# Kernel optimization log

Measured on AMD Instinct MI355X. Metric: run time of the kernel, lower is better.

## Reference

```python
import jax, jax.numpy as jnp
import numpy as np

N_NODES = 50000  # 4 node types x 12500
N_PER = 12500
E = 600000
H = 128
IN_DIMS = [128, 128, 64, 64]


def setup_inputs() -> dict:
    key = jax.random.key(0)
    ks = jax.random.split(key, 16)
    inp = {}
    for i, d in enumerate(IN_DIMS):
        inp[f"feat{i}"] = jax.random.normal(ks[i], (N_PER, d), dtype=jnp.float32)
        # xavier_normal-ish init, gain 1.414
        std = 1.414 * np.sqrt(2.0 / (d + H))
        inp[f"W_fc{i}"] = jax.random.normal(ks[4 + i], (d, H), dtype=jnp.float32) * std
        inp[f"b_fc{i}"] = jnp.zeros((H,), dtype=jnp.float32)
    inp["src"] = jax.random.randint(ks[8], (E,), 0, N_NODES, dtype=jnp.int32)
    inp["dst"] = jax.random.randint(ks[9], (E,), 0, N_NODES, dtype=jnp.int32)
    inp["e_feat"] = jax.random.randint(ks[10], (E,), 0, 36, dtype=jnp.int32)
    inp["b_g0"] = jnp.zeros((H,), dtype=jnp.float32)  # GraphConv layer0 (weight=False, bias)
    inp["W_g1"] = jax.random.normal(ks[11], (H, H), dtype=jnp.float32) * np.sqrt(1.0 / H)
    inp["b_g1"] = jnp.zeros((H,), dtype=jnp.float32)
    return inp


def _degree_norms(src, dst):
    ones = jnp.ones((src.shape[0],), dtype=jnp.float32)
    deg_out = jax.ops.segment_sum(ones, src, num_segments=N_NODES)
    deg_in = jax.ops.segment_sum(ones, dst, num_segments=N_NODES)
    # DGL norm='both': D_out^{-1/2} on src side, D_in^{-1/2} on dst side (clamp 0-degree)
    out_norm = jax.lax.rsqrt(jnp.maximum(deg_out, 1.0))
    in_norm = jax.lax.rsqrt(jnp.maximum(deg_in, 1.0))
    return out_norm, in_norm


def _gcn_aggregate(h, src, dst, out_norm, in_norm):
    m = (h * out_norm[:, None])[src]                      # [E, H] gather
    agg = jax.ops.segment_sum(m, dst, num_segments=N_NODES)
    return agg * in_norm[:, None]


def reference(feat0, feat1, feat2, feat3,
              W_fc0, b_fc0, W_fc1, b_fc1, W_fc2, b_fc2, W_fc3, b_fc3,
              src, dst, e_feat, b_g0, W_g1, b_g1):
    # per-node-type linear projections, then concat along node dim
    h = jnp.concatenate([
        feat0 @ W_fc0 + b_fc0,
        feat1 @ W_fc1 + b_fc1,
        feat2 @ W_fc2 + b_fc2,
        feat3 @ W_fc3 + b_fc3,
    ], axis=0)  # [N_NODES, H]

    out_norm, in_norm = _degree_norms(src, dst)
    # GraphConv layer 0: weight=False, bias, activation (dropout p=0 -> identity)
    h = jax.nn.relu(_gcn_aggregate(h, src, dst, out_norm, in_norm) + b_g0)
    # GraphConv layer 1: aggregate, then linear weight + bias, activation
    h = jax.nn.relu(_gcn_aggregate(h, src, dst, out_norm, in_norm) @ W_g1 + b_g1)

    e = e_feat.astype(jnp.float32)  # e_feat.reshape(-1,1).float() in original
    # forward graph: msg = ft + sum_{r in 0..4} where(e==r, ft, 0) = ft * (1 + 1{e in 0..4})
    w_fwd = 1.0 + sum((e == float(r)).astype(jnp.float32) for r in (0, 1, 2, 3, 4))
    agg_a = jax.ops.segment_sum(h[src] * w_fwd[:, None], dst, num_segments=N_NODES)
    # transpose graph (reversed edges, same e): msg = sum_{r in {6,14,30}} where(e==r, ft, 0)
    w_bwd = sum((e == float(r)).astype(jnp.float32) for r in (6, 14, 30))
    agg_b = jax.ops.segment_sum(h[dst] * w_bwd[:, None], src, num_segments=N_NODES)
    return agg_a + agg_b
```

## Files before the change

kernel.cpp:

```cpp
#include <hip/hip_runtime.h>
#include <hip/hip_bf16.h>

#define N_NODES 50000
#define N_PER   12500
#define E_EDGES 600000
#define HDIM    128

#define NBLK_FC    ((N_PER + 63) / 64)
#define NBLK_G     ((N_NODES + 63) / 64)
#define NBLK_NODE  ((N_NODES + 255) / 256)
#define MASK31  0x7fffffff

#define HQD 64
#define HSL_D (E_EDGES / HQD)
#define NBLK_DB (HQD * 4)
#define HQS 32
#define HSL_S (E_EDGES / HQS)
#define NBLK_S (HQS * 4)

typedef __attribute__((ext_vector_type(8))) short bfrag;
typedef __attribute__((ext_vector_type(4))) float ffrag;

__device__ __forceinline__ unsigned short f2bf(float f) {
    union { float f; unsigned u; } x; x.f = f;
    unsigned r = x.u + 0x7fffu + ((x.u >> 16) & 1u);
    return (unsigned short)(r >> 16);
}
__device__ __forceinline__ float lo_bf(unsigned v) { return __uint_as_float(v << 16); }
__device__ __forceinline__ float hi_bf(unsigned v) { return __uint_as_float(v & 0xffff0000u); }
__device__ __forceinline__ unsigned pack2(float a, float b) {
    return (unsigned)f2bf(a) | ((unsigned)f2bf(b) << 16);
}
__device__ __forceinline__ float onrm_of(int deg) {
    return rsqrtf(fmaxf((float)deg, 1.0f));
}

__device__ __forceinline__ void acc8_add(float* acc, uint4 v) {
    acc[0] += lo_bf(v.x); acc[1] += hi_bf(v.x);
    acc[2] += lo_bf(v.y); acc[3] += hi_bf(v.y);
    acc[4] += lo_bf(v.z); acc[5] += hi_bf(v.z);
    acc[6] += lo_bf(v.w); acc[7] += hi_bf(v.w);
}
__device__ __forceinline__ void acc8_addw(float* acc, uint4 v, float w) {
    acc[0] += lo_bf(v.x) * w; acc[1] += hi_bf(v.x) * w;
    acc[2] += lo_bf(v.y) * w; acc[3] += hi_bf(v.y) * w;
    acc[4] += lo_bf(v.z) * w; acc[5] += hi_bf(v.z) * w;
    acc[6] += lo_bf(v.w) * w; acc[7] += hi_bf(v.w) * w;
}

__global__ __launch_bounds__(256) void prep_kernel(
    const float* __restrict__ W0, const float* __restrict__ W1,
    const float* __restrict__ W2, const float* __restrict__ W3,
    const float* __restrict__ Wg,
    const int* __restrict__ src, const int* __restrict__ dst,
    const int* __restrict__ ef,
    unsigned short* __restrict__ Wp,
    unsigned short* __restrict__ partialS,
    unsigned short* __restrict__ partialD,
    unsigned char*  __restrict__ partialB) {
    __shared__ unsigned hist[N_PER];
    int b = blockIdx.x;
    if (b < NBLK_DB) {
        const int q = b >> 2;
        const int p = b & 3;
        const int g0 = p * N_PER;
        for (int j = threadIdx.x; j < N_PER; j += 256) hist[j] = 0;
        __syncthreads();
        const int e0 = q * HSL_D;
        for (int i = e0 + threadIdx.x; i < e0 + HSL_D; i += 256) {
            int d = dst[i], t = ef[i], s = src[i];
            unsigned rd = (unsigned)(d - g0);
            if (rd < (unsigned)N_PER) atomicAdd(&hist[rd], 1u);
            if (t == 6 || t == 14 || t == 30) {
                unsigned rs = (unsigned)(s - g0);
                if (rs < (unsigned)N_PER) atomicAdd(&hist[rs], 0x10000u);
            }
        }
        __syncthreads();
        for (int j = threadIdx.x; j < N_PER; j += 256) {
            unsigned h = hist[j];
            partialD[(size_t)q * N_NODES + g0 + j] = (unsigned short)(h & 0xffffu);
            partialB[(size_t)q * N_NODES + g0 + j] = (unsigned char)(h >> 16);
        }
    } else if (b < NBLK_DB + NBLK_S) {
        const int r = b - NBLK_DB;
        const int q = r >> 2;
        const int p = r & 3;
        const int g0 = p * N_PER;
        for (int j = threadIdx.x; j < N_PER; j += 256) hist[j] = 0;
        __syncthreads();
        const int e0 = q * HSL_S;
        for (int i = e0 + threadIdx.x; i < e0 + HSL_S; i += 256) {
            unsigned rr = (unsigned)(src[i] - g0);
            if (rr < (unsigned)N_PER) atomicAdd(&hist[rr], 1u);
        }
        __syncthreads();
        for (int j = threadIdx.x; j < N_PER; j += 256)
            partialS[(size_t)q * N_NODES + g0 + j] = (unsigned short)hist[j];
    } else {
        int tid = (b - (NBLK_DB + NBLK_S)) * 256 + threadIdx.x;
        const float* W; int D, base, off;
        if      (tid < 2048) { W = W0; D = 128; base = 0;    off = 0;     }
        else if (tid < 4096) { W = W1; D = 128; base = 2048; off = 16384; }
        else if (tid < 5120) { W = W2; D = 64;  base = 4096; off = 32768; }
        else if (tid < 6144) { W = W3; D = 64;  base = 5120; off = 40960; }
        else                 { W = Wg; D = 128; base = 6144; off = 49152; }
        int t2 = tid - base;
        int KT = D / 32;
        int l = t2 & 63;
        int tt = t2 >> 6;
        int kt = tt % KT, n0 = tt / KT;
        int n = n0 * 16 + (l & 15);
        int kb = kt * 32 + (l >> 4) * 8;
#pragma unroll
        for (int j = 0; j < 8; ++j)
            Wp[(size_t)off + (size_t)t2 * 8 + j] = f2bf(W[(size_t)(kb + j) * 128 + n]);
    }
}

__global__ __launch_bounds__(256) void plane_prefix_kernel(
    unsigned short* __restrict__ partialD, unsigned char* __restrict__ partialB,
    const unsigned short* __restrict__ partialS,
    int* __restrict__ degD, int* __restrict__ degB,
    int* __restrict__ scanD, int* __restrict__ scanB,
    int* __restrict__ blocksumD, int* __restrict__ blocksumB,
    float* __restrict__ onrm_buf) {
    const int t = threadIdx.x;
    const int n = blockIdx.x * 256 + t;
    int dD = 0, dB = 0;
    if (n < N_NODES) {
        int run = 0;
#pragma unroll
        for (int q = 0; q < HQD; ++q) {
            size_t ix = (size_t)q * N_NODES + n;
            int c = partialD[ix];
            partialD[ix] = (unsigned short)run;
            run += c;
        }
        dD = run; degD[n] = run;
        run = 0;
#pragma unroll
        for (int q = 0; q < HQD; ++q) {
            size_t ix = (size_t)q * N_NODES + n;
            int c = partialB[ix];
            partialB[ix] = (unsigned char)run;
            run += c;
        }
        dB = run; degB[n] = run;
        int dS = 0;
#pragma unroll
        for (int q = 0; q < HQS; ++q)
            dS += partialS[(size_t)q * N_NODES + n];
        onrm_buf[n] = onrm_of(dS);
    }
    __shared__ int sD[256], sB[256];
    sD[t] = dD; sB[t] = dB;
    __syncthreads();
    for (int off = 1; off < 256; off <<= 1) {
        int xD = (t >= off) ? sD[t - off] : 0;
        int xB = (t >= off) ? sB[t - off] : 0;
        __syncthreads();
        sD[t] += xD; sB[t] += xB;
        __syncthreads();
    }
    if (n < N_NODES) {
        scanD[n] = sD[t] - dD;
        scanB[n] = sB[t] - dB;
    }
    if (t == 255) {
        blocksumD[blockIdx.x] = sD[255];
        blocksumB[blockIdx.x] = sB[255];
    }
}

__global__ __launch_bounds__(256) void base_add_kernel(
    const int* __restrict__ blocksumD, const int* __restrict__ blocksumB,
    int* __restrict__ scanD, int* __restrict__ scanB) {
    __shared__ int sD[256], sB[256];
    const int t = threadIdx.x;
    const int bid = blockIdx.x;
    sD[t] = (t < bid) ? blocksumD[t] : 0;
    sB[t] = (t < bid) ? blocksumB[t] : 0;
    __syncthreads();
    for (int off = 128; off >= 1; off >>= 1) {
        if (t < off) { sD[t] += sD[t + off]; sB[t] += sB[t + off]; }
        __syncthreads();
    }
    const int n = bid * 256 + t;
    if (n < N_NODES) { scanD[n] += sD[0]; scanB[n] += sB[0]; }
}

__global__ __launch_bounds__(1024) void scatter_kernel(
    const int* __restrict__ src, const int* __restrict__ dst,
    const int* __restrict__ ef,
    const unsigned short* __restrict__ prefD,
    const unsigned char*  __restrict__ prefB,
    const int* __restrict__ scanD, const int* __restrict__ scanB,
    int* __restrict__ bucket, int* __restrict__ bucketB)
{
    __shared__ unsigned offP[N_PER];
    const int b = blockIdx.x;
    const int q = b >> 2;
    const int p = b & 3;
    const int g0 = p * N_PER;
    for (int j = threadIdx.x; j < N_PER; j += 1024)
        offP[j] = (unsigned)(scanD[g0 + j] + (int)prefD[(size_t)q * N_NODES + g0 + j])
                | ((unsigned)prefB[(size_t)q * N_NODES + g0 + j] << 20);
    __syncthreads();
    const int e0 = q * HSL_D;
    for (int i = e0 + threadIdx.x; i < e0 + HSL_D; i += 1024) {
        int s = src[i], d = dst[i], t = ef[i];
        unsigned rd = (unsigned)(d - g0);
        if (rd < (unsigned)N_PER) {
            unsigned old = atomicAdd(&offP[rd], 1u);
            bucket[old & 0xFFFFFu] = s | ((t <= 4) ? 0x80000000 : 0);
        }
        if (t == 6 || t == 14 || t == 30) {
            unsigned rs = (unsigned)(s - g0);
            if (rs < (unsigned)N_PER) {
                unsigned old = atomicAdd(&offP[rs], 1u << 20);
                bucketB[scanB[s] + (int)(old >> 20)] = d;
            }
        }
    }
}

template<int D>
__device__ __forceinline__ void fc_body(
    int blk, int tid,
    const float* __restrict__ X,
    const unsigned short* __restrict__ Wp,
    const float* __restrict__ bias,
    const float* __restrict__ onrm,
    unsigned short* __restrict__ outbf,
    int rows)
{
    constexpr int KT = D / 32;
    const int lane = tid & 63;
    const int wave = tid >> 6;
    const int m = lane & 15, q = lane >> 4;
    const int rbase = blk * 64 + wave * 16;
    const int row = rbase + m;

    bfrag afr[KT];
#pragma unroll
    for (int kt = 0; kt < KT; ++kt) {
        bfrag a;
        if (row < rows) {
            const float* xp = X + (size_t)row * D + kt * 32 + q * 8;
            float4 u0 = *(const float4*)xp;
            float4 u1 = *(const float4*)(xp + 4);
            a[0] = (short)f2bf(u0.x); a[1] = (short)f2bf(u0.y);
            a[2] = (short)f2bf(u0.z); a[3] = (short)f2bf(u0.w);
            a[4] = (short)f2bf(u1.x); a[5] = (short)f2bf(u1.y);
            a[6] = (short)f2bf(u1.z); a[7] = (short)f2bf(u1.w);
        } else {
#pragma unroll
            for (int t = 0; t < 8; ++t) a[t] = 0;
        }
        afr[kt] = a;
    }

    ffrag acc[8];
#pragma unroll
    for (int n0 = 0; n0 < 8; ++n0)
#pragma unroll
        for (int t = 0; t < 4; ++t) acc[n0][t] = 0.f;

#pragma unroll
    for (int n0 = 0; n0 < 8; ++n0)
#pragma unroll
        for (int kt = 0; kt < KT; ++kt) {
            bfrag bfr = *(const bfrag*)(Wp + ((size_t)(n0 * KT + kt) * 64 + lane) * 8);
            acc[n0] = __builtin_amdgcn_mfma_f32_16x16x32_bf16(afr[kt], bfr, acc[n0], 0, 0, 0);
        }

#pragma unroll
    for (int n0 = 0; n0 < 8; ++n0) {
        const int col = n0 * 16 + m;
        const float bj = bias[col];
#pragma unroll
        for (int r = 0; r < 4; ++r) {
            int orow = rbase + q * 4 + r;
            if (orow < rows)
                outbf[(size_t)orow * 128 + col] =
                    f2bf((acc[n0][r] + bj) * onrm[orow]);
        }
    }
}

__global__ __launch_bounds__(256) void fc_kernel(
    const float* __restrict__ f0, const float* __restrict__ f1,
    const float* __restrict__ f2, const float* __restrict__ f3,
    const unsigned short* __restrict__ Wp,
    const float* __restrict__ b0, const float* __restrict__ b1,
    const float* __restrict__ b2, const float* __restrict__ b3,
    const float* __restrict__ onrm_buf,
    unsigned short* __restrict__ Abf)
{
    int fb = blockIdx.x;
    int which = fb / NBLK_FC;
    int blk = fb - which * NBLK_FC;
    if (which == 0)
        fc_body<128>(blk, threadIdx.x, f0, Wp,         b0, onrm_buf,
                     Abf + (size_t)0 * N_PER * HDIM, N_PER);
    else if (which == 1)
        fc_body<128>(blk, threadIdx.x, f1, Wp + 16384, b1, onrm_buf + N_PER,
                     Abf + (size_t)1 * N_PER * HDIM, N_PER);
    else if (which == 2)
        fc_body<64>(blk, threadIdx.x, f2, Wp + 32768, b2, onrm_buf + 2 * N_PER,
                    Abf + (size_t)2 * N_PER * HDIM, N_PER);
    else
        fc_body<64>(blk, threadIdx.x, f3, Wp + 40960, b3, onrm_buf + 3 * N_PER,
                    Abf + (size_t)3 * N_PER * HDIM, N_PER);
}

__global__ __launch_bounds__(256) void agg0_kernel(
    const uint4* __restrict__ A,
    const int* __restrict__ bucket, const int* __restrict__ scanD,
    const int* __restrict__ degD,
    const float* __restrict__ onrm_buf, const float* __restrict__ b_g0,
    uint4* __restrict__ B) {
    int idx = blockIdx.x * blockDim.x + threadIdx.x;
    int n = idx >> 4, j8 = idx & 15;
    const int cnt = degD[n];
    const int* bk = bucket + scanD[n];
    float acc[8] = {0.f, 0.f, 0.f, 0.f, 0.f, 0.f, 0.f, 0.f};
    int i = 0;
    for (; i + 4 <= cnt; i += 4) {
        int s0 = bk[i] & MASK31,     s1 = bk[i + 1] & MASK31;
        int s2 = bk[i + 2] & MASK31, s3 = bk[i + 3] & MASK31;
        uint4 v0 = A[(size_t)s0 * 16 + j8];
        uint4 v1 = A[(size_t)s1 * 16 + j8];
        uint4 v2 = A[(size_t)s2 * 16 + j8];
        uint4 v3 = A[(size_t)s3 * 16 + j8];
        acc8_add(acc, v0); acc8_add(acc, v1);
        acc8_add(acc, v2); acc8_add(acc, v3);
    }
    for (; i < cnt; ++i) {
        int s = bk[i] & MASK31;
        acc8_add(acc, A[(size_t)s * 16 + j8]);
    }
    float inr = onrm_of(cnt);
    float onr = onrm_buf[n];
    const float* bg = b_g0 + j8 * 8;
    float r[8];
#pragma unroll
    for (int k = 0; k < 8; ++k)
        r[k] = fmaxf(acc[k] * inr + bg[k], 0.f) * onr;
    uint4 o;
    o.x = pack2(r[0], r[1]); o.y = pack2(r[2], r[3]);
    o.z = pack2(r[4], r[5]); o.w = pack2(r[6], r[7]);
    B[(size_t)n * 16 + j8] = o;
}

__global__ __launch_bounds__(256) void gemmg_kernel(
    const unsigned short* __restrict__ Bbf,
    const unsigned short* __restrict__ Wp,
    unsigned short* __restrict__ BWbf)
{
    const int lane = threadIdx.x & 63;
    const int wave = threadIdx.x >> 6;
    const int m = lane & 15, q = lane >> 4;
    const int rbase = blockIdx.x * 64 + wave * 16;
    const int row = rbase + m;

    bfrag afr[4];
#pragma unroll
    for (int kt = 0; kt < 4; ++kt) {
        if (row < N_NODES)
            afr[kt] = *(const bfrag*)(Bbf + (size_t)row * 128 + kt * 32 + q * 8);
        else {
#pragma unroll
            for (int t = 0; t < 8; ++t) afr[kt][t] = 0;
        }
    }

    ffrag acc[8];
#pragma unroll
    for (int n0 = 0; n0 < 8; ++n0)
#pragma unroll
        for (int t = 0; t < 4; ++t) acc[n0][t] = 0.f;

#pragma unroll
    for (int n0 = 0; n0 < 8; ++n0)
#pragma unroll
        for (int kt = 0; kt < 4; ++kt) {
            bfrag bfr = *(const bfrag*)(Wp + ((size_t)(n0 * 4 + kt) * 64 + lane) * 8);
            acc[n0] = __builtin_amdgcn_mfma_f32_16x16x32_bf16(afr[kt], bfr, acc[n0], 0, 0, 0);
        }

#pragma unroll
    for (int n0 = 0; n0 < 8; ++n0) {
        const int col = n0 * 16 + m;
#pragma unroll
        for (int r = 0; r < 4; ++r) {
            int orow = rbase + q * 4 + r;
            if (orow < N_NODES)
                BWbf[(size_t)orow * 128 + col] = f2bf(acc[n0][r]);
        }
    }
}

__global__ __launch_bounds__(256) void agg1_kernel(
    const uint4* __restrict__ BW,
    const int* __restrict__ bucket, const int* __restrict__ scanD,
    const int* __restrict__ degD,
    const float* __restrict__ b_g1,
    uint4* __restrict__ H) {
    int idx = blockIdx.x * blockDim.x + threadIdx.x;
    int n = idx >> 4, j8 = idx & 15;
    const int cnt = degD[n];
    const int* bk = bucket + scanD[n];
    float acc[8] = {0.f, 0.f, 0.f, 0.f, 0.f, 0.f, 0.f, 0.f};
    int i = 0;
    for (; i + 4 <= cnt; i += 4) {
        int s0 = bk[i] & MASK31,     s1 = bk[i + 1] & MASK31;
        int s2 = bk[i + 2] & MASK31, s3 = bk[i + 3] & MASK31;
        uint4 v0 = BW[(size_t)s0 * 16 + j8];
        uint4 v1 = BW[(size_t)s1 * 16 + j8];
        uint4 v2 = BW[(size_t)s2 * 16 + j8];
        uint4 v3 = BW[(size_t)s3 * 16 + j8];
        acc8_add(acc, v0); acc8_add(acc, v1);
        acc8_add(acc, v2); acc8_add(acc, v3);
    }
    for (; i < cnt; ++i) {
        int s = bk[i] & MASK31;
        acc8_add(acc, BW[(size_t)s * 16 + j8]);
    }
    float inr = onrm_of(cnt);
    const float* bg = b_g1 + j8 * 8;
    float r[8];
#pragma unroll
    for (int k = 0; k < 8; ++k)
        r[k] = fmaxf(acc[k] * inr + bg[k], 0.f);
    uint4 o;
    o.x = pack2(r[0], r[1]); o.y = pack2(r[2], r[3]);
    o.z = pack2(r[4], r[5]); o.w = pack2(r[6], r[7]);
    H[(size_t)n * 16 + j8] = o;
}

__global__ __launch_bounds__(256) void final_kernel(
    const uint4* __restrict__ H,
    const int* __restrict__ bucket, const int* __restrict__ scanD,
    const int* __restrict__ degD,
    const int* __restrict__ bucketB, const int* __restrict__ scanB,
    const int* __restrict__ degB,
    float4* __restrict__ out4) {
    int idx = blockIdx.x * blockDim.x + threadIdx.x;
    int n = idx >> 4, j8 = idx & 15;
    float acc[8] = {0.f, 0.f, 0.f, 0.f, 0.f, 0.f, 0.f, 0.f};
    const int cnt = degD[n];
    const int* bk = bucket + scanD[n];
    int i = 0;
    for (; i + 4 <= cnt; i += 4) {
        int c0 = bk[i], c1 = bk[i + 1], c2 = bk[i + 2], c3 = bk[i + 3];
        uint4 v0 = H[(size_t)(c0 & MASK31) * 16 + j8];
        uint4 v1 = H[(size_t)(c1 & MASK31) * 16 + j8];
        uint4 v2 = H[(size_t)(c2 & MASK31) * 16 + j8];
        uint4 v3 = H[(size_t)(c3 & MASK31) * 16 + j8];
        acc8_addw(acc, v0, (c0 < 0) ? 2.0f : 1.0f);
        acc8_addw(acc, v1, (c1 < 0) ? 2.0f : 1.0f);
        acc8_addw(acc, v2, (c2 < 0) ? 2.0f : 1.0f);
        acc8_addw(acc, v3, (c3 < 0) ? 2.0f : 1.0f);
    }
    for (; i < cnt; ++i) {
        int c = bk[i];
        acc8_addw(acc, H[(size_t)(c & MASK31) * 16 + j8], (c < 0) ? 2.0f : 1.0f);
    }
    const int cb = degB[n];
    const int* bkB = bucketB + scanB[n];
    for (int k = 0; k < cb; ++k) {
        int d = bkB[k];
        acc8_add(acc, H[(size_t)d * 16 + j8]);
    }
    float4 o0 = {acc[0], acc[1], acc[2], acc[3]};
    float4 o1 = {acc[4], acc[5], acc[6], acc[7]};
    out4[(size_t)n * 32 + j8 * 2]     = o0;
    out4[(size_t)n * 32 + j8 * 2 + 1] = o1;
}

extern "C" void kernel_launch(void* const* d_in, const int* in_sizes, int n_in,
                              void* d_out, int out_size, void* d_ws, size_t ws_size,
                              hipStream_t stream) {
    const float* feat[4]  = {(const float*)d_in[0], (const float*)d_in[3],
                             (const float*)d_in[6], (const float*)d_in[9]};
    const float* W_fc[4]  = {(const float*)d_in[1], (const float*)d_in[4],
                             (const float*)d_in[7], (const float*)d_in[10]};
    const float* b_fc[4]  = {(const float*)d_in[2], (const float*)d_in[5],
                             (const float*)d_in[8], (const float*)d_in[11]};
    const int*   src      = (const int*)d_in[12];
    const int*   dst      = (const int*)d_in[13];
    const int*   efeat    = (const int*)d_in[14];
    const float* b_g0     = (const float*)d_in[15];
    const float* W_g1     = (const float*)d_in[16];
    const float* b_g1     = (const float*)d_in[17];
    float* out = (float*)d_out;

    char* p = (char*)d_ws;
    unsigned short* Abf = (unsigned short*)p; p += (size_t)N_NODES * HDIM * 2;
    unsigned short* Bbf = (unsigned short*)p; p += (size_t)N_NODES * HDIM * 2;
    unsigned short* Wp  = (unsigned short*)p; p += (size_t)65536 * 2;
    int* bucket  = (int*)p; p += (size_t)E_EDGES * 4;
    int* bucketB = (int*)p; p += (size_t)E_EDGES * 4;
    unsigned short* partialS = (unsigned short*)p; p += (size_t)HQS * N_NODES * 2;
    unsigned short* partialD = (unsigned short*)p; p += (size_t)HQD * N_NODES * 2;
    unsigned char*  partialB = (unsigned char*)p;  p += (size_t)HQD * N_NODES;
    int* degD  = (int*)p; p += (size_t)N_NODES * 4;
    int* degB  = (int*)p; p += (size_t)N_NODES * 4;
    int* scanD = (int*)p; p += (size_t)N_NODES * 4;
    int* scanB = (int*)p; p += (size_t)N_NODES * 4;
    float* onrm_buf = (float*)p; p += (size_t)N_NODES * 4;
    int* blocksumD = (int*)p; p += 256 * 4;
    int* blocksumB = (int*)p; p += 256 * 4;

    const unsigned short* Wpg = Wp + 49152;

    prep_kernel<<<NBLK_DB + NBLK_S + 32, 256, 0, stream>>>(
        W_fc[0], W_fc[1], W_fc[2], W_fc[3], W_g1, src, dst, efeat,
        Wp, partialS, partialD, partialB);

    plane_prefix_kernel<<<NBLK_NODE, 256, 0, stream>>>(
        partialD, partialB, partialS, degD, degB, scanD, scanB,
        blocksumD, blocksumB, onrm_buf);

    base_add_kernel<<<NBLK_NODE, 256, 0, stream>>>(
        blocksumD, blocksumB, scanD, scanB);

    scatter_kernel<<<NBLK_DB, 1024, 0, stream>>>(
        src, dst, efeat, partialD, partialB, scanD, scanB, bucket, bucketB);

    fc_kernel<<<4 * NBLK_FC, 256, 0, stream>>>(
        feat[0], feat[1], feat[2], feat[3], Wp,
        b_fc[0], b_fc[1], b_fc[2], b_fc[3], onrm_buf, Abf);

    const int grid_node = (N_NODES * 16) / 256;

    agg0_kernel<<<grid_node, 256, 0, stream>>>(
        (const uint4*)Abf, bucket, scanD, degD, onrm_buf, b_g0, (uint4*)Bbf);

    gemmg_kernel<<<NBLK_G, 256, 0, stream>>>(Bbf, Wpg, Abf);

    agg1_kernel<<<grid_node, 256, 0, stream>>>(
        (const uint4*)Abf, bucket, scanD, degD, b_g1, (uint4*)Bbf);

    final_kernel<<<grid_node, 256, 0, stream>>>(
        (const uint4*)Bbf, bucket, scanD, degD, bucketB, scanB, degB, (float4*)out);
}
```

Before: 258.8 us.

## Fold source-degree histogram into dst pass, fuse scatter with FC, deepen gather unroll

The prep kernel no longer runs separate source-degree histogram blocks. Each 32-bit shared histogram word now packs three counts: 10 bits for the dst count, 6 bits for the backward count and 16 bits for the src count, so one pass over the edges fills all three partial arrays. The bucket scatter and the per-type FC projection become one 1024-thread launch, with each FC block running four 256-thread sub-tiles, which removes a kernel boundary and lets the two phases overlap. The gather loops in the three aggregation kernels go from 4 to 8 loads in flight to raise memory-level parallelism. The risks are count overflow in the narrow bit fields, shared-memory conflicts if fc_body assumes a 256-thread block, and lower occupancy from the 50 KB shared array now allocated in every fused block.

Result: faster. 253.0 us (-2.3%).

```diff
diff --git a/kernel.cpp b/kernel.cpp
--- a/kernel.cpp
+++ b/kernel.cpp
@@ -14,9 +14,6 @@
 #define HQD 64
 #define HSL_D (E_EDGES / HQD)
 #define NBLK_DB (HQD * 4)
-#define HQS 32
-#define HSL_S (E_EDGES / HQS)
-#define NBLK_S (HQS * 4)
 
 typedef __attribute__((ext_vector_type(8))) short bfrag;
 typedef __attribute__((ext_vector_type(4))) float ffrag;
@@ -71,34 +68,22 @@
             int d = dst[i], t = ef[i], s = src[i];
             unsigned rd = (unsigned)(d - g0);
             if (rd < (unsigned)N_PER) atomicAdd(&hist[rd], 1u);
-            if (t == 6 || t == 14 || t == 30) {
-                unsigned rs = (unsigned)(s - g0);
-                if (rs < (unsigned)N_PER) atomicAdd(&hist[rs], 0x10000u);
+            unsigned rs = (unsigned)(s - g0);
+            if (rs < (unsigned)N_PER) {
+                unsigned inc = 0x10000u
+                             + ((t == 6 || t == 14 || t == 30) ? 0x400u : 0u);
+                atomicAdd(&hist[rs], inc);
             }
         }
         __syncthreads();
         for (int j = threadIdx.x; j < N_PER; j += 256) {
             unsigned h = hist[j];
-            partialD[(size_t)q * N_NODES + g0 + j] = (unsigned short)(h & 0xffffu);
-            partialB[(size_t)q * N_NODES + g0 + j] = (unsigned char)(h >> 16);
-        }
-    } else if (b < NBLK_DB + NBLK_S) {
-        const int r = b - NBLK_DB;
-        const int q = r >> 2;
-        const int p = r & 3;
-        const int g0 = p * N_PER;
-        for (int j = threadIdx.x; j < N_PER; j += 256) hist[j] = 0;
-        __syncthreads();
-        const int e0 = q * HSL_S;
-        for (int i = e0 + threadIdx.x; i < e0 + HSL_S; i += 256) {
-            unsigned rr = (unsigned)(src[i] - g0);
-            if (rr < (unsigned)N_PER) atomicAdd(&hist[rr], 1u);
-        }
-        __syncthreads();
-        for (int j = threadIdx.x; j < N_PER; j += 256)
-            partialS[(size_t)q * N_NODES + g0 + j] = (unsigned short)hist[j];
+            partialD[(size_t)q * N_NODES + g0 + j] = (unsigned short)(h & 0x3FFu);
+            partialB[(size_t)q * N_NODES + g0 + j] = (unsigned char)((h >> 10) & 0x3Fu);
+            partialS[(size_t)q * N_NODES + g0 + j] = (unsigned short)(h >> 16);
+        }
     } else {
-        int tid = (b - (NBLK_DB + NBLK_S)) * 256 + threadIdx.x;
+        int tid = (b - NBLK_DB) * 256 + threadIdx.x;
         const float* W; int D, base, off;
         if      (tid < 2048) { W = W0; D = 128; base = 0;    off = 0;     }
         else if (tid < 4096) { W = W1; D = 128; base = 2048; off = 16384; }
@@ -149,7 +134,7 @@
         dB = run; degB[n] = run;
         int dS = 0;
 #pragma unroll
-        for (int q = 0; q < HQS; ++q)
+        for (int q = 0; q < HQD; ++q)
             dS += partialS[(size_t)q * N_NODES + n];
         onrm_buf[n] = onrm_of(dS);
     }
@@ -188,41 +173,6 @@
     }
     const int n = bid * 256 + t;
     if (n < N_NODES) { scanD[n] += sD[0]; scanB[n] += sB[0]; }
-}
-
-__global__ __launch_bounds__(1024) void scatter_kernel(
-    const int* __restrict__ src, const int* __restrict__ dst,
-    const int* __restrict__ ef,
-    const unsigned short* __restrict__ prefD,
-    const unsigned char*  __restrict__ prefB,
-    const int* __restrict__ scanD, const int* __restrict__ scanB,
-    int* __restrict__ bucket, int* __restrict__ bucketB)
-{
-    __shared__ unsigned offP[N_PER];
-    const int b = blockIdx.x;
-    const int q = b >> 2;
-    const int p = b & 3;
-    const int g0 = p * N_PER;
-    for (int j = threadIdx.x; j < N_PER; j += 1024)
-        offP[j] = (unsigned)(scanD[g0 + j] + (int)prefD[(size_t)q * N_NODES + g0 + j])
-                | ((unsigned)prefB[(size_t)q * N_NODES + g0 + j] << 20);
-    __syncthreads();
-    const int e0 = q * HSL_D;
-    for (int i = e0 + threadIdx.x; i < e0 + HSL_D; i += 1024) {
-        int s = src[i], d = dst[i], t = ef[i];
-        unsigned rd = (unsigned)(d - g0);
-        if (rd < (unsigned)N_PER) {
-            unsigned old = atomicAdd(&offP[rd], 1u);
-            bucket[old & 0xFFFFFu] = s | ((t <= 4) ? 0x80000000 : 0);
-        }
-        if (t == 6 || t == 14 || t == 30) {
-            unsigned rs = (unsigned)(s - g0);
-            if (rs < (unsigned)N_PER) {
-                unsigned old = atomicAdd(&offP[rs], 1u << 20);
-                bucketB[scanB[s] + (int)(old >> 20)] = d;
-            }
-        }
-    }
 }
 
 template<int D>
@@ -289,7 +239,13 @@
     }
 }
 
-__global__ __launch_bounds__(256) void fc_kernel(
+__global__ __launch_bounds__(1024) void scatfc_kernel(
+    const int* __restrict__ src, const int* __restrict__ dst,
+    const int* __restrict__ ef,
+    const unsigned short* __restrict__ prefD,
+    const unsigned char*  __restrict__ prefB,
+    const int* __restrict__ scanD, const int* __restrict__ scanB,
+    int* __restrict__ bucket, int* __restrict__ bucketB,
     const float* __restrict__ f0, const float* __restrict__ f1,
     const float* __restrict__ f2, const float* __restrict__ f3,
     const unsigned short* __restrict__ Wp,
@@ -298,21 +254,50 @@
     const float* __restrict__ onrm_buf,
     unsigned short* __restrict__ Abf)
 {
-    int fb = blockIdx.x;
-    int which = fb / NBLK_FC;
-    int blk = fb - which * NBLK_FC;
-    if (which == 0)
-        fc_body<128>(blk, threadIdx.x, f0, Wp,         b0, onrm_buf,
-                     Abf + (size_t)0 * N_PER * HDIM, N_PER);
-    else if (which == 1)
-        fc_body<128>(blk, threadIdx.x, f1, Wp + 16384, b1, onrm_buf + N_PER,
-                     Abf + (size_t)1 * N_PER * HDIM, N_PER);
-    else if (which == 2)
-        fc_body<64>(blk, threadIdx.x, f2, Wp + 32768, b2, onrm_buf + 2 * N_PER,
-                    Abf + (size_t)2 * N_PER * HDIM, N_PER);
-    else
-        fc_body<64>(blk, threadIdx.x, f3, Wp + 40960, b3, onrm_buf + 3 * N_PER,
-                    Abf + (size_t)3 * N_PER * HDIM, N_PER);
+    __shared__ unsigned offP[N_PER];
+    const int b = blockIdx.x;
+    if (b < NBLK_DB) {
+        const int q = b >> 2;
+        const int p = b & 3;
+        const int g0 = p * N_PER;
+        for (int j = threadIdx.x; j < N_PER; j += 1024)
+            offP[j] = (unsigned)(scanD[g0 + j] + (int)prefD[(size_t)q * N_NODES + g0 + j])
+                    | ((unsigned)prefB[(size_t)q * N_NODES + g0 + j] << 20);
+        __syncthreads();
+        const int e0 = q * HSL_D;
+        for (int i = e0 + threadIdx.x; i < e0 + HSL_D; i += 1024) {
+            int s = src[i], d = dst[i], t = ef[i];
+            unsigned rd = (unsigned)(d - g0);
+            if (rd < (unsigned)N_PER) {
+                unsigned old = atomicAdd(&offP[rd], 1u);
+                bucket[old & 0xFFFFFu] = s | ((t <= 4) ? 0x80000000 : 0);
+            }
+            if (t == 6 || t == 14 || t == 30) {
+                unsigned rs = (unsigned)(s - g0);
+                if (rs < (unsigned)N_PER) {
+                    unsigned old = atomicAdd(&offP[rs], 1u << 20);
+                    bucketB[scanB[s] + (int)(old >> 20)] = d;
+                }
+            }
+        }
+    } else {
+        int ft = (b - NBLK_DB) * 4 + (threadIdx.x >> 8);
+        int tid = threadIdx.x & 255;
+        int which = ft / NBLK_FC;
+        int blk = ft - which * NBLK_FC;
+        if (which == 0)
+            fc_body<128>(blk, tid, f0, Wp,         b0, onrm_buf,
+                         Abf + (size_t)0 * N_PER * HDIM, N_PER);
+        else if (which == 1)
+            fc_body<128>(blk, tid, f1, Wp + 16384, b1, onrm_buf + N_PER,
+                         Abf + (size_t)1 * N_PER * HDIM, N_PER);
+        else if (which == 2)
+            fc_body<64>(blk, tid, f2, Wp + 32768, b2, onrm_buf + 2 * N_PER,
+                        Abf + (size_t)2 * N_PER * HDIM, N_PER);
+        else
+            fc_body<64>(blk, tid, f3, Wp + 40960, b3, onrm_buf + 3 * N_PER,
+                        Abf + (size_t)3 * N_PER * HDIM, N_PER);
+    }
 }
 
 __global__ __launch_bounds__(256) void agg0_kernel(
@@ -327,20 +312,25 @@
     const int* bk = bucket + scanD[n];
     float acc[8] = {0.f, 0.f, 0.f, 0.f, 0.f, 0.f, 0.f, 0.f};
     int i = 0;
-    for (; i + 4 <= cnt; i += 4) {
-        int s0 = bk[i] & MASK31,     s1 = bk[i + 1] & MASK31;
-        int s2 = bk[i + 2] & MASK31, s3 = bk[i + 3] & MASK31;
-        uint4 v0 = A[(size_t)s0 * 16 + j8];
-        uint4 v1 = A[(size_t)s1 * 16 + j8];
-        uint4 v2 = A[(size_t)s2 * 16 + j8];
-        uint4 v3 = A[(size_t)s3 * 16 + j8];
-        acc8_add(acc, v0); acc8_add(acc, v1);
-        acc8_add(acc, v2); acc8_add(acc, v3);
-    }
-    for (; i < cnt; ++i) {
-        int s = bk[i] & MASK31;
-        acc8_add(acc, A[(size_t)s * 16 + j8]);
-    }
+    for (; i + 8 <= cnt; i += 8) {
+        uint4 v[8];
+#pragma unroll
+        for (int k = 0; k < 8; ++k)
+            v[k] = A[(size_t)(bk[i + k] & MASK31) * 16 + j8];
+#pragma unroll
+        for (int k = 0; k < 8; ++k) acc8_add(acc, v[k]);
+    }
+    if (i + 4 <= cnt) {
+        uint4 v[4];
+#pragma unroll
+        for (int k = 0; k < 4; ++k)
+            v[k] = A[(size_t)(bk[i + k] & MASK31) * 16 + j8];
+#pragma unroll
+        for (int k = 0; k < 4; ++k) acc8_add(acc, v[k]);
+        i += 4;
+    }
+    for (; i < cnt; ++i)
+        acc8_add(acc, A[(size_t)(bk[i] & MASK31) * 16 + j8]);
     float inr = onrm_of(cnt);
     float onr = onrm_buf[n];
     const float* bg = b_g0 + j8 * 8;
@@ -414,20 +404,25 @@
     const int* bk = bucket + scanD[n];
     float acc[8] = {0.f, 0.f, 0.f, 0.f, 0.f, 0.f, 0.f, 0.f};
     int i = 0;
-    for (; i + 4 <= cnt; i += 4) {
-        int s0 = bk[i] & MASK31,     s1 = bk[i + 1] & MASK31;
-        int s2 = bk[i + 2] & MASK31, s3 = bk[i + 3] & MASK31;
-        uint4 v0 = BW[(size_t)s0 * 16 + j8];
-        uint4 v1 = BW[(size_t)s1 * 16 + j8];
-        uint4 v2 = BW[(size_t)s2 * 16 + j8];
-        uint4 v3 = BW[(size_t)s3 * 16 + j8];
-        acc8_add(acc, v0); acc8_add(acc, v1);
-        acc8_add(acc, v2); acc8_add(acc, v3);
-    }
-    for (; i < cnt; ++i) {
-        int s = bk[i] & MASK31;
-        acc8_add(acc, BW[(size_t)s * 16 + j8]);
-    }
+    for (; i + 8 <= cnt; i += 8) {
+        uint4 v[8];
+#pragma unroll
+        for (int k = 0; k < 8; ++k)
+            v[k] = BW[(size_t)(bk[i + k] & MASK31) * 16 + j8];
+#pragma unroll
+        for (int k = 0; k < 8; ++k) acc8_add(acc, v[k]);
+    }
+    if (i + 4 <= cnt) {
+        uint4 v[4];
+#pragma unroll
+        for (int k = 0; k < 4; ++k)
+            v[k] = BW[(size_t)(bk[i + k] & MASK31) * 16 + j8];
+#pragma unroll
+        for (int k = 0; k < 4; ++k) acc8_add(acc, v[k]);
+        i += 4;
+    }
+    for (; i < cnt; ++i)
+        acc8_add(acc, BW[(size_t)(bk[i] & MASK31) * 16 + j8]);
     float inr = onrm_of(cnt);
     const float* bg = b_g1 + j8 * 8;
     float r[8];
@@ -453,16 +448,28 @@
     const int cnt = degD[n];
     const int* bk = bucket + scanD[n];
     int i = 0;
-    for (; i + 4 <= cnt; i += 4) {
-        int c0 = bk[i], c1 = bk[i + 1], c2 = bk[i + 2], c3 = bk[i + 3];
-        uint4 v0 = H[(size_t)(c0 & MASK31) * 16 + j8];
-        uint4 v1 = H[(size_t)(c1 & MASK31) * 16 + j8];
-        uint4 v2 = H[(size_t)(c2 & MASK31) * 16 + j8];
-        uint4 v3 = H[(size_t)(c3 & MASK31) * 16 + j8];
-        acc8_addw(acc, v0, (c0 < 0) ? 2.0f : 1.0f);
-        acc8_addw(acc, v1, (c1 < 0) ? 2.0f : 1.0f);
-        acc8_addw(acc, v2, (c2 < 0) ? 2.0f : 1.0f);
-        acc8_addw(acc, v3, (c3 < 0) ? 2.0f : 1.0f);
+    for (; i + 8 <= cnt; i += 8) {
+        int c[8]; uint4 v[8];
+#pragma unroll
+        for (int k = 0; k < 8; ++k) c[k] = bk[i + k];
+#pragma unroll
+        for (int k = 0; k < 8; ++k)
+            v[k] = H[(size_t)(c[k] & MASK31) * 16 + j8];
+#pragma unroll
+        for (int k = 0; k < 8; ++k)
+            acc8_addw(acc, v[k], (c[k] < 0) ? 2.0f : 1.0f);
+    }
+    if (i + 4 <= cnt) {
+        int c[4]; uint4 v[4];
+#pragma unroll
+        for (int k = 0; k < 4; ++k) c[k] = bk[i + k];
+#pragma unroll
+        for (int k = 0; k < 4; ++k)
+            v[k] = H[(size_t)(c[k] & MASK31) * 16 + j8];
+#pragma unroll
+        for (int k = 0; k < 4; ++k)
+            acc8_addw(acc, v[k], (c[k] < 0) ? 2.0f : 1.0f);
+        i += 4;
     }
     for (; i < cnt; ++i) {
         int c = bk[i];
@@ -503,7 +510,7 @@
     unsigned short* Wp  = (unsigned short*)p; p += (size_t)65536 * 2;
     int* bucket  = (int*)p; p += (size_t)E_EDGES * 4;
     int* bucketB = (int*)p; p += (size_t)E_EDGES * 4;
-    unsigned short* partialS = (unsigned short*)p; p += (size_t)HQS * N_NODES * 2;
+    unsigned short* partialS = (unsigned short*)p; p += (size_t)HQD * N_NODES * 2;
     unsigned short* partialD = (unsigned short*)p; p += (size_t)HQD * N_NODES * 2;
     unsigned char*  partialB = (unsigned char*)p;  p += (size_t)HQD * N_NODES;
     int* degD  = (int*)p; p += (size_t)N_NODES * 4;
@@ -516,7 +523,7 @@
 
     const unsigned short* Wpg = Wp + 49152;
 
-    prep_kernel<<<NBLK_DB + NBLK_S + 32, 256, 0, stream>>>(
+    prep_kernel<<<NBLK_DB + 32, 256, 0, stream>>>(
         W_fc[0], W_fc[1], W_fc[2], W_fc[3], W_g1, src, dst, efeat,
         Wp, partialS, partialD, partialB);
 
@@ -527,10 +534,8 @@
     base_add_kernel<<<NBLK_NODE, 256, 0, stream>>>(
         blocksumD, blocksumB, scanD, scanB);
 
-    scatter_kernel<<<NBLK_DB, 1024, 0, stream>>>(
-        src, dst, efeat, partialD, partialB, scanD, scanB, bucket, bucketB);
-
-    fc_kernel<<<4 * NBLK_FC, 256, 0, stream>>>(
+    scatfc_kernel<<<NBLK_DB + NBLK_FC, 1024, 0, stream>>>(
+        src, dst, efeat, partialD, partialB, scanD, scanB, bucket, bucketB,
         feat[0], feat[1], feat[2], feat[3], Wp,
         b_fc[0], b_fc[1], b_fc[2], b_fc[3], onrm_buf, Abf);
 
```
